# Performance work log

Hardware: AMD Instinct MI355X
Metric: run time of the kernel (lower is better)

Reference implementation:

```python
import jax, jax.numpy as jnp
import numpy as np

B, S, H, NH, I, V, P, T = 8, 512, 768, 12, 3072, 30522, 512, 2
D = H // NH
EPS = 1e-12


def _ln(x, g, b):
    m = x.mean(-1, keepdims=True)
    v = ((x - m) ** 2).mean(-1, keepdims=True)
    return (x - m) / jnp.sqrt(v + EPS) * g + b


def setup_inputs() -> dict:
    key = jax.random.key(0)
    ks = jax.random.split(key, 24)
    s = 0.02
    f32 = jnp.float32
    d = {
        'x': jax.random.randint(ks[0], (B, S), 0, V, dtype=jnp.int32),
        'W_word': (jax.random.normal(ks[1], (V, H)) * s).astype(f32),
        'W_pos': (jax.random.normal(ks[2], (P, H)) * s).astype(f32),
        'W_type': (jax.random.normal(ks[3], (T, H)) * s).astype(f32),
        'g_emb': jnp.ones((H,), f32), 'b_emb': jnp.zeros((H,), f32),
        'Wq': (jax.random.normal(ks[4], (H, H)) * s).astype(f32), 'bq': jnp.zeros((H,), f32),
        'Wk': (jax.random.normal(ks[5], (H, H)) * s).astype(f32), 'bk': jnp.zeros((H,), f32),
        'Wv': (jax.random.normal(ks[6], (H, H)) * s).astype(f32), 'bv': jnp.zeros((H,), f32),
        'Wo': (jax.random.normal(ks[7], (H, H)) * s).astype(f32), 'bo': jnp.zeros((H,), f32),
        'g_attn': jnp.ones((H,), f32), 'b_attn': jnp.zeros((H,), f32),
        'Wi': (jax.random.normal(ks[8], (H, I)) * s).astype(f32), 'bi': jnp.zeros((I,), f32),
        'Wd': (jax.random.normal(ks[9], (I, H)) * s).astype(f32), 'bd': jnp.zeros((H,), f32),
        'g_out': jnp.ones((H,), f32), 'b_out': jnp.zeros((H,), f32),
        'Wp': (jax.random.normal(ks[10], (H, H)) * s).astype(f32), 'bp': jnp.zeros((H,), f32),
    }
    return d


def _forward(x, W_word, W_pos, W_type, g_emb, b_emb, Wq, bq, Wk, bk, Wv, bv,
             Wo, bo, g_attn, b_attn, Wi, bi, Wd, bd, g_out, b_out, Wp, bp):
    # embeddings: word + position(arange) + token_type(all zeros -> row 0)
    h = W_word[x] + W_pos[jnp.arange(S)][None, :, :] + W_type[0][None, None, :]
    h = _ln(h, g_emb, b_emb)
    scale = 1.0 / jnp.sqrt(jnp.float32(D))
    # NOTE: the torch module shares one set of layer weights across all 6 layers.
    for _ in range(6):
        q = (h @ Wq + bq).reshape(B, S, NH, D).transpose(0, 2, 1, 3)  # bhsd
        k = (h @ Wk + bk).reshape(B, S, NH, D).transpose(0, 2, 1, 3)
        v = (h @ Wv + bv).reshape(B, S, NH, D).transpose(0, 2, 1, 3)
        scores = jnp.einsum('bhqd,bhkd->bhqk', q, k) * scale
        probs = jax.nn.softmax(scores, axis=-1)
        ctx = jnp.einsum('bhqk,bhkd->bhqd', probs, v)
        ctx = ctx.transpose(0, 2, 1, 3).reshape(B, S, H)
        attn = ctx @ Wo + bo
        xa = _ln(h + attn, g_attn, b_attn)
        ff = jax.nn.gelu(xa @ Wi + bi, approximate=False) @ Wd + bd
        h = _ln(xa + ff, g_out, b_out)
    pooled = h[:, 0, :] @ Wp + bp  # no tanh in the original module
    return h, pooled


def reference(x, W_word, W_pos, W_type, g_emb, b_emb, Wq, bq, Wk, bk, Wv, bv,
              Wo, bo, g_attn, b_attn, Wi, bi, Wd, bd, g_out, b_out, Wp, bp):
    return _forward(x, W_word, W_pos, W_type, g_emb, b_emb, Wq, bq, Wk, bk, Wv, bv,
                    Wo, bo, g_attn, b_attn, Wi, bi, Wd, bd, g_out, b_out, Wp, bp)
```

## Files before the change

### kernel.cpp

```cpp
#include <hip/hip_runtime.h>
#include <hip/hip_bf16.h>
#include <math.h>

#define B_  8
#define S_  512
#define H_  768
#define NH_ 12
#define D_  64
#define I_  3072
#define NTOK (B_*S_)
#define LDQ 2304

typedef __attribute__((ext_vector_type(8))) __bf16 bf16x8;
typedef __attribute__((ext_vector_type(8))) unsigned short ushort8;
typedef __attribute__((ext_vector_type(4))) float  f32x4;

__device__ __forceinline__ float gelu_exact(float x) {
    return 0.5f * x * (1.0f + erff(x * 0.70710678118654752440f));
}

__device__ __forceinline__ unsigned short f2bf(float x) {
    __hip_bfloat16 h = __float2bfloat16(x);
    return *reinterpret_cast<unsigned short*>(&h);
}

__device__ __forceinline__ void gload16(const void* g, void* l) {
    __builtin_amdgcn_global_load_lds(
        (const __attribute__((address_space(1))) void*)g,
        (__attribute__((address_space(3))) void*)l,
        16, 0, 0);
}

__global__ void cvtT_kernel(const float* __restrict__ W, __hip_bfloat16* __restrict__ WT,
                            int K, int N) {
    __shared__ float tile[32][33];
    int k0 = blockIdx.y * 32, n0 = blockIdx.x * 32;
    int tx = threadIdx.x & 31, ty = threadIdx.x >> 5;
    #pragma unroll
    for (int i = 0; i < 32; i += 8)
        tile[ty + i][tx] = W[(long)(k0 + ty + i) * N + n0 + tx];
    __syncthreads();
    #pragma unroll
    for (int i = 0; i < 32; i += 8)
        WT[(long)(n0 + ty + i) * K + k0 + tx] = __float2bfloat16(tile[tx][ty + i]);
}

__global__ void embed_ln_kernel(const int* __restrict__ ids,
                                const float* __restrict__ Wword,
                                const float* __restrict__ Wpos,
                                const float* __restrict__ Wtype,
                                const float* __restrict__ g,
                                const float* __restrict__ b,
                                float* __restrict__ out,
                                __hip_bfloat16* __restrict__ outb) {
    int t = blockIdx.x;
    int s = t % S_;
    long id = ids[t];
    int tid = threadIdx.x;
    float vals[3];
    float sum = 0.f, sq = 0.f;
    #pragma unroll
    for (int i = 0; i < 3; ++i) {
        int c = tid + 256 * i;
        float e = Wword[id * H_ + c] + Wpos[(long)s * H_ + c] + Wtype[c];
        vals[i] = e; sum += e; sq += e * e;
    }
    __shared__ float r1[256], r2[256];
    r1[tid] = sum; r2[tid] = sq; __syncthreads();
    for (int st = 128; st > 0; st >>= 1) {
        if (tid < st) { r1[tid] += r1[tid + st]; r2[tid] += r2[tid + st]; }
        __syncthreads();
    }
    float mean = r1[0] * (1.0f / H_);
    float var  = r2[0] * (1.0f / H_) - mean * mean;
    float inv  = rsqrtf(var + 1e-12f);
    #pragma unroll
    for (int i = 0; i < 3; ++i) {
        int c = tid + 256 * i;
        float v = (vals[i] - mean) * inv * g[c] + b[c];
        out[(long)t * H_ + c] = v;
        outb[(long)t * H_ + c] = __float2bfloat16(v);
    }
}

__global__ void add_ln_kernel(const float* __restrict__ a,
                              const float* __restrict__ r,
                              const float* __restrict__ g,
                              const float* __restrict__ bb,
                              float* __restrict__ out,
                              __hip_bfloat16* __restrict__ outb) {
    int t = blockIdx.x;
    int tid = threadIdx.x;
    float vals[3];
    float sum = 0.f, sq = 0.f;
    #pragma unroll
    for (int i = 0; i < 3; ++i) {
        int c = tid + 256 * i;
        float e = a[(long)t * H_ + c] + r[(long)t * H_ + c];
        vals[i] = e; sum += e; sq += e * e;
    }
    __shared__ float r1[256], r2[256];
    r1[tid] = sum; r2[tid] = sq; __syncthreads();
    for (int st = 128; st > 0; st >>= 1) {
        if (tid < st) { r1[tid] += r1[tid + st]; r2[tid] += r2[tid + st]; }
        __syncthreads();
    }
    float mean = r1[0] * (1.0f / H_);
    float var  = r2[0] * (1.0f / H_) - mean * mean;
    float inv  = rsqrtf(var + 1e-12f);
    #pragma unroll
    for (int i = 0; i < 3; ++i) {
        int c = tid + 256 * i;
        float v = (vals[i] - mean) * inv * g[c] + bb[c];
        out[(long)t * H_ + c] = v;
        outb[(long)t * H_ + c] = __float2bfloat16(v);
    }
}

template<int BM, int BN, int MI, int NJ, int ACT, int WF32, int WB16>
__global__ __launch_bounds__(256, 2) void mfma_gemm_kernel(
    const __hip_bfloat16* __restrict__ A,
    const __hip_bfloat16* __restrict__ BT,
    const float* __restrict__ bias,
    float* __restrict__ Cf,
    __hip_bfloat16* __restrict__ Cb,
    int M, int N, int K) {
    constexpr int WC = BN / (NJ * 16);
    constexpr int WR = BM / (MI * 16);
    static_assert(WR * WC == 4, "4 waves");
    __shared__ __align__(16) __hip_bfloat16 sA[BM * 32];
    __shared__ __align__(16) __hip_bfloat16 sB[BN * 32];
    const int tid  = threadIdx.x;
    const int lane = tid & 63;
    const int w    = tid >> 6;
    const int wr   = w / WC, wc = w % WC;
    const int l15  = lane & 15, l4 = lane >> 4;
    const int m0 = blockIdx.y * BM, n0 = blockIdx.x * BN;

    f32x4 acc[MI][NJ] = {};

    for (int k0 = 0; k0 < K; k0 += 32) {
        #pragma unroll
        for (int t = 0; t < BM * 4 / 256; ++t) {
            int c = tid + 256 * t;
            gload16(A + (long)(m0 + (c >> 2)) * K + k0 + (c & 3) * 8, sA + c * 8);
        }
        #pragma unroll
        for (int t = 0; t < BN * 4 / 256; ++t) {
            int c = tid + 256 * t;
            gload16(BT + (long)(n0 + (c >> 2)) * K + k0 + (c & 3) * 8, sB + c * 8);
        }
        __syncthreads();
        const int kk = l4 * 8;
        bf16x8 af[MI], bf[NJ];
        #pragma unroll
        for (int i = 0; i < MI; ++i)
            af[i] = *reinterpret_cast<const bf16x8*>(sA + (wr * MI * 16 + i * 16 + l15) * 32 + kk);
        #pragma unroll
        for (int j = 0; j < NJ; ++j)
            bf[j] = *reinterpret_cast<const bf16x8*>(sB + (wc * NJ * 16 + j * 16 + l15) * 32 + kk);
        #pragma unroll
        for (int i = 0; i < MI; ++i)
            #pragma unroll
            for (int j = 0; j < NJ; ++j)
                acc[i][j] = __builtin_amdgcn_mfma_f32_16x16x32_bf16(af[i], bf[j], acc[i][j], 0, 0, 0);
        __syncthreads();
    }

    #pragma unroll
    for (int i = 0; i < MI; ++i) {
        #pragma unroll
        for (int j = 0; j < NJ; ++j) {
            int col = n0 + wc * NJ * 16 + j * 16 + l15;
            float bv = bias[col];
            #pragma unroll
            for (int r = 0; r < 4; ++r) {
                int row = m0 + wr * MI * 16 + i * 16 + l4 * 4 + r;
                float v = acc[i][j][r] + bv;
                if (ACT == 1) v = gelu_exact(v);
                if (WF32) Cf[(long)row * N + col] = v;
                if (WB16) Cb[(long)row * N + col] = __float2bfloat16(v);
            }
        }
    }
}

__global__ __launch_bounds__(256, 4) void flash_attn_kernel(
    const __hip_bfloat16* __restrict__ QKV,
    __hip_bfloat16* __restrict__ Ctx) {
    __shared__ __align__(16) unsigned short sK[64 * 72];
    __shared__ __align__(16) unsigned short sVt[64 * 72];
    __shared__ __align__(16) unsigned short sP[4 * 16 * 72];

    const int tid  = threadIdx.x;
    const int lane = tid & 63;
    const int w    = tid >> 6;
    const int l15  = lane & 15, l4 = lane >> 4;
    const int qb = blockIdx.x;
    const int bh = blockIdx.y;
    const int b  = bh / NH_, hd = bh % NH_;
    const long rbase = (long)b * S_ * LDQ;
    const int qoff = hd * D_, koff = H_ + hd * D_, voff = 2 * H_ + hd * D_;

    const int qrow0 = qb * 64 + w * 16;
    bf16x8 af[2];
    #pragma unroll
    for (int ks = 0; ks < 2; ++ks)
        af[ks] = *reinterpret_cast<const bf16x8*>(
            QKV + rbase + (long)(qrow0 + l15) * LDQ + qoff + ks * 32 + l4 * 8);

    f32x4 ctx[4] = {};
    float m_run[4], l_run[4];
    #pragma unroll
    for (int r = 0; r < 4; ++r) { m_run[r] = -1e30f; l_run[r] = 0.f; }

    const int sr = tid >> 2;
    const int sc = (tid & 3) * 16;
    unsigned short* pl = sP + w * (16 * 72);

    for (int kv0 = 0; kv0 < S_; kv0 += 64) {
        const __hip_bfloat16* kg = QKV + rbase + (long)(kv0 + sr) * LDQ + koff + sc;
        const __hip_bfloat16* vg = QKV + rbase + (long)(kv0 + sr) * LDQ + voff + sc;
        ushort8 kv_a = *reinterpret_cast<const ushort8*>(kg);
        ushort8 kv_b = *reinterpret_cast<const ushort8*>(kg + 8);
        ushort8 vv_a = *reinterpret_cast<const ushort8*>(vg);
        ushort8 vv_b = *reinterpret_cast<const ushort8*>(vg + 8);
        __syncthreads();
        *reinterpret_cast<ushort8*>(sK + sr * 72 + sc)     = kv_a;
        *reinterpret_cast<ushort8*>(sK + sr * 72 + sc + 8) = kv_b;
        #pragma unroll
        for (int i = 0; i < 8; ++i) {
            sVt[(sc + i) * 72 + sr]     = vv_a[i];
            sVt[(sc + 8 + i) * 72 + sr] = vv_b[i];
        }
        __syncthreads();

        f32x4 s[4];
        #pragma unroll
        for (int j = 0; j < 4; ++j) {
            s[j] = (f32x4){0.f, 0.f, 0.f, 0.f};
            #pragma unroll
            for (int ks = 0; ks < 2; ++ks) {
                bf16x8 bk = *reinterpret_cast<const bf16x8*>(sK + (j * 16 + l15) * 72 + ks * 32 + l4 * 8);
                s[j] = __builtin_amdgcn_mfma_f32_16x16x32_bf16(af[ks], bk, s[j], 0, 0, 0);
            }
        }
        #pragma unroll
        for (int j = 0; j < 4; ++j) s[j] *= 0.125f;

        #pragma unroll
        for (int r = 0; r < 4; ++r) {
            float mx = fmaxf(fmaxf(s[0][r], s[1][r]), fmaxf(s[2][r], s[3][r]));
            #pragma unroll
            for (int o = 1; o < 16; o <<= 1) mx = fmaxf(mx, __shfl_xor(mx, o));
            float mnew = fmaxf(m_run[r], mx);
            float sum = 0.f;
            #pragma unroll
            for (int j = 0; j < 4; ++j) {
                float p = __expf(s[j][r] - mnew);
                s[j][r] = p; sum += p;
            }
            #pragma unroll
            for (int o = 1; o < 16; o <<= 1) sum += __shfl_xor(sum, o);
            float resc = __expf(m_run[r] - mnew);
            l_run[r] = l_run[r] * resc + sum;
            m_run[r] = mnew;
            #pragma unroll
            for (int j = 0; j < 4; ++j) ctx[j][r] *= resc;
        }

        #pragma unroll
        for (int j = 0; j < 4; ++j)
            #pragma unroll
            for (int r = 0; r < 4; ++r)
                pl[(l4 * 4 + r) * 72 + j * 16 + l15] = f2bf(s[j][r]);

        #pragma unroll
        for (int ks = 0; ks < 2; ++ks) {
            bf16x8 ap = *reinterpret_cast<const bf16x8*>(pl + l15 * 72 + ks * 32 + l4 * 8);
            #pragma unroll
            for (int jd = 0; jd < 4; ++jd) {
                bf16x8 bv = *reinterpret_cast<const bf16x8*>(sVt + (jd * 16 + l15) * 72 + ks * 32 + l4 * 8);
                ctx[jd] = __builtin_amdgcn_mfma_f32_16x16x32_bf16(ap, bv, ctx[jd], 0, 0, 0);
            }
        }
    }

    #pragma unroll
    for (int r = 0; r < 4; ++r) {
        float inv = 1.f / l_run[r];
        long tok = (long)b * S_ + qb * 64 + w * 16 + l4 * 4 + r;
        #pragma unroll
        for (int jd = 0; jd < 4; ++jd)
            Ctx[tok * H_ + hd * D_ + jd * 16 + l15] = __float2bfloat16(ctx[jd][r] * inv);
    }
}

__global__ void pooled_kernel(const float* __restrict__ h,
                              const float* __restrict__ Wp,
                              const float* __restrict__ bp,
                              float* __restrict__ out) {
    int b = blockIdx.y;
    int col = blockIdx.x * 256 + threadIdx.x;
    const float* hb = h + (long)b * S_ * H_;
    float acc = 0.f;
    #pragma unroll 8
    for (int k = 0; k < H_; ++k)
        acc += hb[k] * Wp[(long)k * H_ + col];
    out[(long)b * H_ + col] = acc + bp[col];
}

extern "C" void kernel_launch(void* const* d_in, const int* in_sizes, int n_in,
                              void* d_out, int out_size, void* d_ws, size_t ws_size,
                              hipStream_t stream) {
    const int*   x      = (const int*)  d_in[0];
    const float* W_word = (const float*)d_in[1];
    const float* W_pos  = (const float*)d_in[2];
    const float* W_type = (const float*)d_in[3];
    const float* g_emb  = (const float*)d_in[4];
    const float* b_emb  = (const float*)d_in[5];
    const float* Wq     = (const float*)d_in[6];
    const float* bq     = (const float*)d_in[7];
    const float* Wk     = (const float*)d_in[8];
    const float* bk     = (const float*)d_in[9];
    const float* Wv     = (const float*)d_in[10];
    const float* bv     = (const float*)d_in[11];
    const float* Wo     = (const float*)d_in[12];
    const float* bo     = (const float*)d_in[13];
    const float* g_attn = (const float*)d_in[14];
    const float* b_attn = (const float*)d_in[15];
    const float* Wi     = (const float*)d_in[16];
    const float* bi     = (const float*)d_in[17];
    const float* Wd     = (const float*)d_in[18];
    const float* bd     = (const float*)d_in[19];
    const float* g_out  = (const float*)d_in[20];
    const float* b_out  = (const float*)d_in[21];
    const float* Wp     = (const float*)d_in[22];
    const float* bp     = (const float*)d_in[23];

    const size_t NT = (size_t)NTOK * H_;
    char* base = (char*)d_ws;
    size_t off = 0;
    auto alloc = [&](size_t bytes) -> char* {
        char* p = base + off;
        off += (bytes + 255) & ~(size_t)255;
        return p;
    };
    float* h    = (float*)alloc(NT * 4);
    float* xa   = (float*)alloc(NT * 4);
    float* kb   = (float*)alloc(NT * 4);
    __hip_bfloat16* h_b   = (__hip_bfloat16*)alloc(NT * 2);
    __hip_bfloat16* xa_b  = (__hip_bfloat16*)alloc(NT * 2);
    __hip_bfloat16* qkv_b = (__hip_bfloat16*)alloc((size_t)NTOK * LDQ * 2);
    __hip_bfloat16* ctx_b = (__hip_bfloat16*)alloc(NT * 2);
    __hip_bfloat16* ff1_b = (__hip_bfloat16*)alloc((size_t)NTOK * I_ * 2);
    __hip_bfloat16* WqkvT = (__hip_bfloat16*)alloc((size_t)LDQ * H_ * 2);
    __hip_bfloat16* WoT = (__hip_bfloat16*)alloc((size_t)H_ * H_ * 2);
    __hip_bfloat16* WiT = (__hip_bfloat16*)alloc((size_t)H_ * I_ * 2);
    __hip_bfloat16* WdT = (__hip_bfloat16*)alloc((size_t)I_ * H_ * 2);
    float* bqkv = (float*)alloc(LDQ * 4);

    cvtT_kernel<<<dim3(H_/32, H_/32), 256, 0, stream>>>(Wq, WqkvT, H_, H_);
    cvtT_kernel<<<dim3(H_/32, H_/32), 256, 0, stream>>>(Wk, WqkvT + (size_t)H_ * H_, H_, H_);
    cvtT_kernel<<<dim3(H_/32, H_/32), 256, 0, stream>>>(Wv, WqkvT + (size_t)2 * H_ * H_, H_, H_);
    cvtT_kernel<<<dim3(H_/32, H_/32), 256, 0, stream>>>(Wo, WoT, H_, H_);
    cvtT_kernel<<<dim3(I_/32, H_/32), 256, 0, stream>>>(Wi, WiT, H_, I_);
    cvtT_kernel<<<dim3(H_/32, I_/32), 256, 0, stream>>>(Wd, WdT, I_, H_);
    hipMemcpyAsync(bqkv,          bq, H_ * 4, hipMemcpyDeviceToDevice, stream);
    hipMemcpyAsync(bqkv + H_,     bk, H_ * 4, hipMemcpyDeviceToDevice, stream);
    hipMemcpyAsync(bqkv + 2 * H_, bv, H_ * 4, hipMemcpyDeviceToDevice, stream);

    embed_ln_kernel<<<NTOK, 256, 0, stream>>>(x, W_word, W_pos, W_type, g_emb, b_emb, h, h_b);

    dim3 gqkv(LDQ/128, NTOK/128);
    dim3 g768(H_/64,  NTOK/128);
    dim3 gi(I_/128,  NTOK/128);
    for (int layer = 0; layer < 6; ++layer) {
        mfma_gemm_kernel<128,128,4,4,0,0,1><<<gqkv, 256, 0, stream>>>(
            h_b, WqkvT, bqkv, nullptr, qkv_b, NTOK, LDQ, H_);
        flash_attn_kernel<<<dim3(S_/64, B_*NH_), 256, 0, stream>>>(qkv_b, ctx_b);
        mfma_gemm_kernel<128,64,4,2,0,1,0><<<g768, 256, 0, stream>>>(
            ctx_b, WoT, bo, kb, nullptr, NTOK, H_, H_);
        add_ln_kernel<<<NTOK, 256, 0, stream>>>(h, kb, g_attn, b_attn, xa, xa_b);
        mfma_gemm_kernel<128,128,4,4,1,0,1><<<gi, 256, 0, stream>>>(
            xa_b, WiT, bi, nullptr, ff1_b, NTOK, I_, H_);
        mfma_gemm_kernel<128,64,4,2,0,1,0><<<g768, 256, 0, stream>>>(
            ff1_b, WdT, bd, kb, nullptr, NTOK, H_, I_);
        add_ln_kernel<<<NTOK, 256, 0, stream>>>(xa, kb, g_out, b_out, h, h_b);
    }

    hipMemcpyAsync(d_out, h, NT * sizeof(float), hipMemcpyDeviceToDevice, stream);
    pooled_kernel<<<dim3(3, 8), 256, 0, stream>>>(h, Wp, bp, (float*)d_out + NT);
}
```

Before: 1.173 ms.

## Double-buffer shared memory in MFMA GEMM to overlap global loads with compute

Splits the GEMM's shared-memory A/B tiles into two buffers and issues the next k-slice's direct-to-LDS loads before computing on the current one. Uses explicit vmcnt waits and s_barrier in place of __syncthreads, so the in-flight prefetch is not drained before compute. Raises the launch_bounds occupancy hint from 2 to 3 blocks per CU. This costs twice the LDS per block and more register pressure under the higher occupancy target, and it depends on gload16 being an async global-to-LDS load counted by vmcnt.

Result: no change. 1.182 ms (+0.8%).

```diff
diff --git a/kernel.cpp b/kernel.cpp
--- a/kernel.cpp
+++ b/kernel.cpp
@@ -118,7 +118,7 @@
 }
 
 template<int BM, int BN, int MI, int NJ, int ACT, int WF32, int WB16>
-__global__ __launch_bounds__(256, 2) void mfma_gemm_kernel(
+__global__ __launch_bounds__(256, 3) void mfma_gemm_kernel(
     const __hip_bfloat16* __restrict__ A,
     const __hip_bfloat16* __restrict__ BT,
     const float* __restrict__ bias,
@@ -128,8 +128,11 @@
     constexpr int WC = BN / (NJ * 16);
     constexpr int WR = BM / (MI * 16);
     static_assert(WR * WC == 4, "4 waves");
-    __shared__ __align__(16) __hip_bfloat16 sA[BM * 32];
-    __shared__ __align__(16) __hip_bfloat16 sB[BN * 32];
+    constexpr int LA = BM * 4 / 256;
+    constexpr int LB = BN * 4 / 256;
+    constexpr int L  = LA + LB;
+    __shared__ __align__(16) __hip_bfloat16 sA[2][BM * 32];
+    __shared__ __align__(16) __hip_bfloat16 sB[2][BN * 32];
     const int tid  = threadIdx.x;
     const int lane = tid & 63;
     const int w    = tid >> 6;
@@ -137,34 +140,52 @@
     const int l15  = lane & 15, l4 = lane >> 4;
     const int m0 = blockIdx.y * BM, n0 = blockIdx.x * BN;
 
+    auto stage = [&](int buf, int k0) {
+        #pragma unroll
+        for (int t = 0; t < LA; ++t) {
+            int c = tid + 256 * t;
+            gload16(A + (long)(m0 + (c >> 2)) * K + k0 + (c & 3) * 8, &sA[buf][c * 8]);
+        }
+        #pragma unroll
+        for (int t = 0; t < LB; ++t) {
+            int c = tid + 256 * t;
+            gload16(BT + (long)(n0 + (c >> 2)) * K + k0 + (c & 3) * 8, &sB[buf][c * 8]);
+        }
+    };
+
     f32x4 acc[MI][NJ] = {};
-
-    for (int k0 = 0; k0 < K; k0 += 32) {
-        #pragma unroll
-        for (int t = 0; t < BM * 4 / 256; ++t) {
-            int c = tid + 256 * t;
-            gload16(A + (long)(m0 + (c >> 2)) * K + k0 + (c & 3) * 8, sA + c * 8);
-        }
-        #pragma unroll
-        for (int t = 0; t < BN * 4 / 256; ++t) {
-            int c = tid + 256 * t;
-            gload16(BT + (long)(n0 + (c >> 2)) * K + k0 + (c & 3) * 8, sB + c * 8);
-        }
-        __syncthreads();
+    const int nk = K >> 5;
+
+    stage(0, 0);
+    for (int t = 0; t < nk; ++t) {
+        const int cur = t & 1;
+        if (t + 1 < nk) {
+            stage(cur ^ 1, (t + 1) * 32);
+            asm volatile("s_waitcnt vmcnt(%0)" :: "i"(L) : "memory");
+        } else {
+            asm volatile("s_waitcnt vmcnt(0)" ::: "memory");
+        }
+        __builtin_amdgcn_sched_barrier(0);
+        __builtin_amdgcn_s_barrier();
+        __builtin_amdgcn_sched_barrier(0);
+
         const int kk = l4 * 8;
         bf16x8 af[MI], bf[NJ];
         #pragma unroll
         for (int i = 0; i < MI; ++i)
-            af[i] = *reinterpret_cast<const bf16x8*>(sA + (wr * MI * 16 + i * 16 + l15) * 32 + kk);
+            af[i] = *reinterpret_cast<const bf16x8*>(&sA[cur][(wr * MI * 16 + i * 16 + l15) * 32 + kk]);
         #pragma unroll
         for (int j = 0; j < NJ; ++j)
-            bf[j] = *reinterpret_cast<const bf16x8*>(sB + (wc * NJ * 16 + j * 16 + l15) * 32 + kk);
+            bf[j] = *reinterpret_cast<const bf16x8*>(&sB[cur][(wc * NJ * 16 + j * 16 + l15) * 32 + kk]);
         #pragma unroll
         for (int i = 0; i < MI; ++i)
             #pragma unroll
             for (int j = 0; j < NJ; ++j)
                 acc[i][j] = __builtin_amdgcn_mfma_f32_16x16x32_bf16(af[i], bf[j], acc[i][j], 0, 0, 0);
-        __syncthreads();
+
+        __builtin_amdgcn_sched_barrier(0);
+        __builtin_amdgcn_s_barrier();
+        __builtin_amdgcn_sched_barrier(0);
     }
 
     #pragma unroll
```
